# Kernel optimization log

Hardware: AMD Instinct MI355X
Metric: run time of the kernel (lower is better)

Reference implementation:

```python
import jax, jax.numpy as jnp
import numpy as np

EPS = 1e-5

def _layernorm(x, gamma, beta):
    mu = jnp.mean(x, axis=-1, keepdims=True)
    var = jnp.var(x, axis=-1, keepdims=True)
    return (x - mu) * jax.lax.rsqrt(var + EPS) * gamma + beta

def setup_inputs() -> dict:
    key = jax.random.key(0)
    ks = jax.random.split(key, 8)
    B, I, H = 8192, 1024, 1024
    s_w = 1.0 / np.sqrt(I)
    s_u = 1.0 / np.sqrt(H)
    return {
        "x": jax.random.normal(ks[0], (B, I), jnp.float32),
        "h": jax.random.normal(ks[1], (B, H), jnp.float32),
        "c": jax.random.normal(ks[2], (B, H), jnp.float32),
        "W_w": jax.random.uniform(ks[3], (I, 4 * H), jnp.float32, -s_w, s_w),
        "W_b": jax.random.uniform(ks[4], (4 * H,), jnp.float32, -s_w, s_w),
        "U_w": jax.random.uniform(ks[5], (H, 4 * H), jnp.float32, -s_u, s_u),
        "ln_g_gamma": jnp.ones((4 * H,), jnp.float32),
        "ln_g_beta": jnp.zeros((4 * H,), jnp.float32),
        "ln_c_gamma": jnp.ones((H,), jnp.float32),
        "ln_c_beta": jnp.zeros((H,), jnp.float32),
    }

def reference(x, h, c, W_w, W_b, U_w, ln_g_gamma, ln_g_beta, ln_c_gamma, ln_c_beta):
    gates_x = x @ W_w + W_b            # [B, 4H]
    gates_h = h @ U_w                  # [B, 4H]
    gates = gates_x + gates_h + gates_x * gates_h  # multiplicative integration
    gates = _layernorm(gates, ln_g_gamma, ln_g_beta)
    i, f, g, o = jnp.split(gates, 4, axis=-1)
    i = jax.nn.sigmoid(i)
    f = jax.nn.sigmoid(f)
    o = jax.nn.sigmoid(o)
    g = jnp.tanh(g)
    c_new = f * c + i * g
    c_new = _layernorm(c_new, ln_c_gamma, ln_c_beta)
    h_new = o * jnp.tanh(c_new)
    return (h_new, h_new, c_new)
```

## Files before the change

kernel.cpp:

```cpp
#include <hip/hip_runtime.h>
#include <cstdint>


#define MB (1024ull * 1024ull)

typedef short bf16x8 __attribute__((ext_vector_type(8)));
typedef float f32x4  __attribute__((ext_vector_type(4)));

__device__ __forceinline__ bool bf16_mode(const void* g1) {
    return ((const unsigned short*)g1)[0] == 0x3F80u;
}
__device__ __forceinline__ float b2f(unsigned short u) {
    union { unsigned int i; float f; } v; v.i = ((unsigned int)u) << 16; return v.f;
}
__device__ __forceinline__ unsigned short f2b(float f) {
    unsigned int i = __float_as_uint(f);
    unsigned int r = (i + 0x7FFFu + ((i >> 16) & 1u)) >> 16;
    return (unsigned short)r;
}
__device__ __forceinline__ void up4(uint2 v, float* o) {
    o[0] = __uint_as_float(v.x << 16);
    o[1] = __uint_as_float(v.x & 0xFFFF0000u);
    o[2] = __uint_as_float(v.y << 16);
    o[3] = __uint_as_float(v.y & 0xFFFF0000u);
}
__device__ __forceinline__ unsigned int pack2(unsigned short a, unsigned short b) {
    return (unsigned int)a | ((unsigned int)b << 16);
}
__device__ __forceinline__ void ld4(const void* p, size_t idx, bool isbf, float* o) {
    if (isbf) up4(*(const uint2*)((const unsigned short*)p + idx), o);
    else { float4 v = *(const float4*)((const float*)p + idx); o[0]=v.x; o[1]=v.y; o[2]=v.z; o[3]=v.w; }
}
__device__ __forceinline__ float fast_sigmoid(float z) { return 1.f / (1.f + __expf(-z)); }
__device__ __forceinline__ float fast_tanh(float z)    { return 1.f - 2.f / (__expf(2.f * z) + 1.f); }

__device__ __forceinline__ void load_lds16(const unsigned short* g, unsigned short* l) {
    __builtin_amdgcn_global_load_lds(
        (const __attribute__((address_space(1))) unsigned int*)g,
        (__attribute__((address_space(3))) unsigned int*)l,
        16, 0, 0);
}

__global__ __launch_bounds__(256)
void prep_weights(const void* __restrict__ src, const void* __restrict__ g1,
                  unsigned short* __restrict__ dst)
{
    const bool isbf = bf16_mode(g1);
    __shared__ unsigned short tile[64][68];
    const int t  = threadIdx.x;
    const int tx = t & 15;
    const int ty = t >> 4;
    const int bx = blockIdx.x * 64;
    const int by = blockIdx.y * 64;
    if (isbf) {
        const unsigned short* s = (const unsigned short*)src;
#pragma unroll
        for (int it = 0; it < 4; ++it) {
            const int r = ty + it * 16;
            uint2 v = *(const uint2*)(s + (size_t)(by + r) * 4096 + bx + tx * 4);
            tile[r][tx * 4 + 0] = (unsigned short)(v.x & 0xFFFFu);
            tile[r][tx * 4 + 1] = (unsigned short)(v.x >> 16);
            tile[r][tx * 4 + 2] = (unsigned short)(v.y & 0xFFFFu);
            tile[r][tx * 4 + 3] = (unsigned short)(v.y >> 16);
        }
    } else {
        const float* s = (const float*)src;
#pragma unroll
        for (int it = 0; it < 4; ++it) {
            const int r = ty + it * 16;
            float4 v = *(const float4*)(s + (size_t)(by + r) * 4096 + bx + tx * 4);
            tile[r][tx * 4 + 0] = f2b(v.x);
            tile[r][tx * 4 + 1] = f2b(v.y);
            tile[r][tx * 4 + 2] = f2b(v.z);
            tile[r][tx * 4 + 3] = f2b(v.w);
        }
    }
    __syncthreads();
#pragma unroll
    for (int it = 0; it < 4; ++it) {
        const int rn = ty + it * 16;
        const int ck = tx * 4;
        uint2 w;
        w.x = pack2(tile[ck + 0][rn], tile[ck + 1][rn]);
        w.y = pack2(tile[ck + 2][rn], tile[ck + 3][rn]);
        *(uint2*)(dst + (size_t)(bx + rn) * 1024 + by + ck) = w;
    }
}

__global__ __launch_bounds__(256)
void prep_xh(const void* __restrict__ X, const void* __restrict__ Hs,
             const void* __restrict__ g1, void* __restrict__ outb)
{
    if (bf16_mode(g1)) return;
    const float* src = (blockIdx.y == 0) ? (const float*)X : (const float*)Hs;
    unsigned short* dst = (unsigned short*)((char*)outb + (blockIdx.y == 0 ? 48 * MB : 80 * MB));
    const size_t i0 = ((size_t)blockIdx.x * 256 + threadIdx.x) * 8;
    float4 a = *(const float4*)(src + i0);
    float4 b = *(const float4*)(src + i0 + 4);
    uint4 o;
    o.x = pack2(f2b(a.x), f2b(a.y));
    o.y = pack2(f2b(a.z), f2b(a.w));
    o.z = pack2(f2b(b.x), f2b(b.y));
    o.w = pack2(f2b(b.z), f2b(b.w));
    *(uint4*)(dst + i0) = o;
}

#define TM 128
#define TN 128
#define TK 32

__global__ __launch_bounds__(256, 2)
void milstm_gemm(const void* __restrict__ Xraw, const void* __restrict__ Hraw,
                 const void* __restrict__ g1, const void* __restrict__ Wbraw,
                 const void* __restrict__ outb,
                 const unsigned short* __restrict__ Wt,
                 const unsigned short* __restrict__ Ut,
                 unsigned short* __restrict__ G, int m0)
{
    const bool isbf = bf16_mode(g1);
    const unsigned short* X  = isbf ? (const unsigned short*)Xraw
                                    : (const unsigned short*)((const char*)outb + 48 * MB);
    const unsigned short* Hs = isbf ? (const unsigned short*)Hraw
                                    : (const unsigned short*)((const char*)outb + 80 * MB);

    __shared__ __align__(16) unsigned short sAx[TM * TK];
    __shared__ __align__(16) unsigned short sAh[TM * TK];
    __shared__ __align__(16) unsigned short sBw[TN * TK];
    __shared__ __align__(16) unsigned short sBu[TN * TK];

    const int tid  = threadIdx.x;
    const int wave = tid >> 6;
    const int lane = tid & 63;
    const int quad = lane >> 4;
    const int l16  = lane & 15;

    const int bm = blockIdx.y * TM;
    const int bn = blockIdx.x * TN;

    const int wm = (wave & 1) * 64;
    const int wn = (wave >> 1) * 64;

    const int c0   = wave * 2;
    const int srow = lane >> 2;
    const int skb  = (lane & 3) ^ ((srow >> 1) & 3);
    const int scol = skb * 8;

    const unsigned short* px0 = X  + (size_t)(m0 + bm + (c0 + 0) * 16 + srow) * 1024 + scol;
    const unsigned short* px1 = X  + (size_t)(m0 + bm + (c0 + 1) * 16 + srow) * 1024 + scol;
    const unsigned short* ph0 = Hs + (size_t)(m0 + bm + (c0 + 0) * 16 + srow) * 1024 + scol;
    const unsigned short* ph1 = Hs + (size_t)(m0 + bm + (c0 + 1) * 16 + srow) * 1024 + scol;
    const unsigned short* pw0 = Wt + (size_t)(bn + (c0 + 0) * 16 + srow) * 1024 + scol;
    const unsigned short* pw1 = Wt + (size_t)(bn + (c0 + 1) * 16 + srow) * 1024 + scol;
    const unsigned short* pu0 = Ut + (size_t)(bn + (c0 + 0) * 16 + srow) * 1024 + scol;
    const unsigned short* pu1 = Ut + (size_t)(bn + (c0 + 1) * 16 + srow) * 1024 + scol;

    unsigned short* dax0 = sAx + (c0 + 0) * 512;
    unsigned short* dax1 = sAx + (c0 + 1) * 512;
    unsigned short* dah0 = sAh + (c0 + 0) * 512;
    unsigned short* dah1 = sAh + (c0 + 1) * 512;
    unsigned short* dbw0 = sBw + (c0 + 0) * 512;
    unsigned short* dbw1 = sBw + (c0 + 1) * 512;
    unsigned short* dbu0 = sBu + (c0 + 0) * 512;
    unsigned short* dbu1 = sBu + (c0 + 1) * 512;

    const int kread = (quad ^ ((l16 >> 1) & 3)) * 8;

    f32x4 accx[4][4] = {};
    f32x4 acch[4][4] = {};

    for (int k0 = 0; k0 < 1024; k0 += TK) {
        load_lds16(px0 + k0, dax0);
        load_lds16(px1 + k0, dax1);
        load_lds16(ph0 + k0, dah0);
        load_lds16(ph1 + k0, dah1);
        load_lds16(pw0 + k0, dbw0);
        load_lds16(pw1 + k0, dbw1);
        load_lds16(pu0 + k0, dbu0);
        load_lds16(pu1 + k0, dbu1);
        __syncthreads();

        bf16x8 ax[4], ah[4];
#pragma unroll
        for (int mi = 0; mi < 4; ++mi) {
            ax[mi] = *(const bf16x8*)(sAx + (wm + mi * 16 + l16) * TK + kread);
            ah[mi] = *(const bf16x8*)(sAh + (wm + mi * 16 + l16) * TK + kread);
        }
#pragma unroll
        for (int ni = 0; ni < 4; ++ni) {
            bf16x8 bw = *(const bf16x8*)(sBw + (wn + ni * 16 + l16) * TK + kread);
            bf16x8 bu = *(const bf16x8*)(sBu + (wn + ni * 16 + l16) * TK + kread);
#pragma unroll
            for (int mi = 0; mi < 4; ++mi) {
                accx[mi][ni] = __builtin_amdgcn_mfma_f32_16x16x32_bf16(ax[mi], bw, accx[mi][ni], 0, 0, 0);
                acch[mi][ni] = __builtin_amdgcn_mfma_f32_16x16x32_bf16(ah[mi], bu, acch[mi][ni], 0, 0, 0);
            }
        }
        __syncthreads();
    }

#pragma unroll
    for (int ni = 0; ni < 4; ++ni) {
        const int col = bn + wn + ni * 16 + l16;
        const float bias = isbf ? b2f(((const unsigned short*)Wbraw)[col])
                                : ((const float*)Wbraw)[col];
#pragma unroll
        for (int mi = 0; mi < 4; ++mi) {
            const int row0 = bm + wm + mi * 16 + quad * 4;
#pragma unroll
            for (int r = 0; r < 4; ++r) {
                float gx = accx[mi][ni][r] + bias;
                float gh = acch[mi][ni][r];
                float gv = gx + gh + gx * gh;
                G[(size_t)(row0 + r) * 4096 + col] = f2b(gv);
            }
        }
    }
}

__global__ __launch_bounds__(256)
void milstm_cell(const unsigned short* __restrict__ G,
                 const void* __restrict__ C,
                 const void* __restrict__ g1, const void* __restrict__ b1,
                 const void* __restrict__ g2, const void* __restrict__ b2,
                 void* __restrict__ outb, int m0)
{
    const bool isbf = bf16_mode(g1);
    const int lrow = blockIdx.x;
    const int row  = m0 + lrow;
    const int tid  = threadIdx.x;
    const int lane = tid & 63;
    const int wave = tid >> 6;
    const unsigned short* grow = G + (size_t)lrow * 4096;

    __shared__ __align__(16) unsigned short srow[4096];
    __shared__ float red[16];

    float s = 0.f, ss = 0.f;
    const uint4* gv4 = (const uint4*)grow;
#pragma unroll
    for (int u = 0; u < 2; ++u) {
        uint4 v = gv4[tid * 2 + u];
        *(uint4*)(srow + (size_t)(tid * 2 + u) * 8) = v;
        unsigned int w[4] = { v.x, v.y, v.z, v.w };
#pragma unroll
        for (int q = 0; q < 4; ++q) {
            float flo = __uint_as_float(w[q] << 16);
            float fhi = __uint_as_float(w[q] & 0xFFFF0000u);
            s  += flo + fhi;
            ss += flo * flo + fhi * fhi;
        }
    }
#pragma unroll
    for (int off = 32; off > 0; off >>= 1) {
        s  += __shfl_xor(s, off, 64);
        ss += __shfl_xor(ss, off, 64);
    }
    if (lane == 0) { red[wave] = s; red[8 + wave] = ss; }
    __syncthreads();
    s  = red[0] + red[1] + red[2] + red[3];
    ss = red[8] + red[9] + red[10] + red[11];
    const float mu   = s * (1.f / 4096.f);
    const float rstd = rsqrtf(fmaxf(ss * (1.f / 4096.f) - mu * mu, 0.f) + 1e-5f);

    const int j0 = tid * 4;
    float xi[4], xf[4], xg[4], xo[4], cc[4];
    float G1[4], B1[4], ii[4], cn[4], ov[4];

    up4(*(const uint2*)(srow + j0),        xi);
    up4(*(const uint2*)(srow + 1024 + j0), xf);
    up4(*(const uint2*)(srow + 2048 + j0), xg);
    up4(*(const uint2*)(srow + 3072 + j0), xo);
    ld4(C, (size_t)row * 1024 + j0, isbf, cc);

    ld4(g1, j0, isbf, G1); ld4(b1, j0, isbf, B1);
#pragma unroll
    for (int q = 0; q < 4; ++q) ii[q] = fast_sigmoid((xi[q] - mu) * rstd * G1[q] + B1[q]);
    ld4(g1, 1024 + j0, isbf, G1); ld4(b1, 1024 + j0, isbf, B1);
#pragma unroll
    for (int q = 0; q < 4; ++q) xf[q] = fast_sigmoid((xf[q] - mu) * rstd * G1[q] + B1[q]);
    ld4(g1, 2048 + j0, isbf, G1); ld4(b1, 2048 + j0, isbf, B1);
#pragma unroll
    for (int q = 0; q < 4; ++q) xg[q] = fast_tanh((xg[q] - mu) * rstd * G1[q] + B1[q]);
    ld4(g1, 3072 + j0, isbf, G1); ld4(b1, 3072 + j0, isbf, B1);
#pragma unroll
    for (int q = 0; q < 4; ++q) ov[q] = fast_sigmoid((xo[q] - mu) * rstd * G1[q] + B1[q]);
#pragma unroll
    for (int q = 0; q < 4; ++q) cn[q] = xf[q] * cc[q] + ii[q] * xg[q];

    float s2  = cn[0] + cn[1] + cn[2] + cn[3];
    float ss2 = cn[0]*cn[0] + cn[1]*cn[1] + cn[2]*cn[2] + cn[3]*cn[3];
#pragma unroll
    for (int off = 32; off > 0; off >>= 1) {
        s2  += __shfl_xor(s2, off, 64);
        ss2 += __shfl_xor(ss2, off, 64);
    }
    if (lane == 0) { red[4 + wave] = s2; red[12 + wave] = ss2; }
    __syncthreads();
    s2  = red[4]  + red[5]  + red[6]  + red[7];
    ss2 = red[12] + red[13] + red[14] + red[15];
    const float mu2   = s2 * (1.f / 1024.f);
    const float rstd2 = rsqrtf(fmaxf(ss2 * (1.f / 1024.f) - mu2 * mu2, 0.f) + 1e-5f);

    ld4(g2, j0, isbf, G1);
    ld4(b2, j0, isbf, B1);

    float hv[4], cv[4];
#pragma unroll
    for (int q = 0; q < 4; ++q) {
        cv[q] = (cn[q] - mu2) * rstd2 * G1[q] + B1[q];
        hv[q] = ov[q] * fast_tanh(cv[q]);
    }

    const size_t BH = (size_t)8192 * 1024;
    if (isbf) {
        unsigned short* out = (unsigned short*)outb;
        uint2 hb, cb;
        hb.x = pack2(f2b(hv[0]), f2b(hv[1])); hb.y = pack2(f2b(hv[2]), f2b(hv[3]));
        cb.x = pack2(f2b(cv[0]), f2b(cv[1])); cb.y = pack2(f2b(cv[2]), f2b(cv[3]));
        *(uint2*)(out + (size_t)row * 1024 + j0)          = hb;
        *(uint2*)(out + BH + (size_t)row * 1024 + j0)     = hb;
        *(uint2*)(out + 2 * BH + (size_t)row * 1024 + j0) = cb;
    } else {
        float* out = (float*)outb;
        float4 hf = { hv[0], hv[1], hv[2], hv[3] };
        float4 cf = { cv[0], cv[1], cv[2], cv[3] };
        *(float4*)(out + (size_t)row * 1024 + j0)          = hf;
        *(float4*)(out + BH + (size_t)row * 1024 + j0)     = hf;
        *(float4*)(out + 2 * BH + (size_t)row * 1024 + j0) = cf;
    }
}

extern "C" void kernel_launch(void* const* d_in, const int* in_sizes, int n_in,
                              void* d_out, int out_size, void* d_ws, size_t ws_size,
                              hipStream_t stream)
{
    const void* X  = d_in[0];
    const void* Hh = d_in[1];
    const void* C  = d_in[2];
    const void* Ww = d_in[3];
    const void* Wb = d_in[4];
    const void* Uw = d_in[5];
    const void* g1 = d_in[6];
    const void* b1 = d_in[7];
    const void* g2 = d_in[8];
    const void* b2 = d_in[9];

    const bool single = ws_size >= 80 * MB;
    const size_t goff = single ? 64 * MB : 32 * MB;
    unsigned short* G  = (unsigned short*)d_ws;
    unsigned short* Wt = (unsigned short*)((char*)d_ws + goff);
    unsigned short* Ut = (unsigned short*)((char*)d_ws + goff + 8 * MB);

    prep_weights<<<dim3(64, 16), 256, 0, stream>>>(Ww, g1, Wt);
    prep_weights<<<dim3(64, 16), 256, 0, stream>>>(Uw, g1, Ut);
    prep_xh<<<dim3(4096, 2), 256, 0, stream>>>(X, Hh, g1, d_out);

    if (single) {
        milstm_gemm<<<dim3(32, 64), 256, 0, stream>>>(X, Hh, g1, Wb, d_out, Wt, Ut, G, 0);
        milstm_cell<<<dim3(8192), 256, 0, stream>>>(G, C, g1, b1, g2, b2, d_out, 0);
    } else {
        for (int ph = 0; ph < 2; ++ph) {
            const int m0 = ph * 4096;
            milstm_gemm<<<dim3(32, 32), 256, 0, stream>>>(X, Hh, g1, Wb, d_out, Wt, Ut, G, m0);
            milstm_cell<<<dim3(4096), 256, 0, stream>>>(G, C, g1, b1, g2, b2, d_out, m0);
        }
    }
}
```

Measured before the change: 399.7 us.

## Halve GEMM N-tile to raise occupancy and drop LDS staging in cell kernel

The GEMM tile shrinks from 128x128 to 128x64 with 3 blocks per CU. The LDS load assignment is rewritten so each wave issues 6 chunk loads spread across X, H, W and U, and the launch grid doubles in N. The cell kernel now reads each thread's gate slices directly from global memory into registers and preloads all gamma/beta values, removing the shared-memory row copy. This trades lower per-block data reuse (A tiles are reloaded twice as often) for more resident waves and better latency hiding.

```diff
diff --git a/kernel.cpp b/kernel.cpp
--- a/kernel.cpp
+++ b/kernel.cpp
@@ -106,10 +106,10 @@
 }
 
 #define TM 128
-#define TN 128
+#define TN 64
 #define TK 32
 
-__global__ __launch_bounds__(256, 2)
+__global__ __launch_bounds__(256, 3)
 void milstm_gemm(const void* __restrict__ Xraw, const void* __restrict__ Hraw,
                  const void* __restrict__ g1, const void* __restrict__ Wbraw,
                  const void* __restrict__ outb,
@@ -138,45 +138,36 @@
     const int bn = blockIdx.x * TN;
 
     const int wm = (wave & 1) * 64;
-    const int wn = (wave >> 1) * 64;
-
-    const int c0   = wave * 2;
+    const int wn = (wave >> 1) * 32;
+
     const int srow = lane >> 2;
     const int skb  = (lane & 3) ^ ((srow >> 1) & 3);
     const int scol = skb * 8;
 
-    const unsigned short* px0 = X  + (size_t)(m0 + bm + (c0 + 0) * 16 + srow) * 1024 + scol;
-    const unsigned short* px1 = X  + (size_t)(m0 + bm + (c0 + 1) * 16 + srow) * 1024 + scol;
-    const unsigned short* ph0 = Hs + (size_t)(m0 + bm + (c0 + 0) * 16 + srow) * 1024 + scol;
-    const unsigned short* ph1 = Hs + (size_t)(m0 + bm + (c0 + 1) * 16 + srow) * 1024 + scol;
-    const unsigned short* pw0 = Wt + (size_t)(bn + (c0 + 0) * 16 + srow) * 1024 + scol;
-    const unsigned short* pw1 = Wt + (size_t)(bn + (c0 + 1) * 16 + srow) * 1024 + scol;
-    const unsigned short* pu0 = Ut + (size_t)(bn + (c0 + 0) * 16 + srow) * 1024 + scol;
-    const unsigned short* pu1 = Ut + (size_t)(bn + (c0 + 1) * 16 + srow) * 1024 + scol;
-
-    unsigned short* dax0 = sAx + (c0 + 0) * 512;
-    unsigned short* dax1 = sAx + (c0 + 1) * 512;
-    unsigned short* dah0 = sAh + (c0 + 0) * 512;
-    unsigned short* dah1 = sAh + (c0 + 1) * 512;
-    unsigned short* dbw0 = sBw + (c0 + 0) * 512;
-    unsigned short* dbw1 = sBw + (c0 + 1) * 512;
-    unsigned short* dbu0 = sBu + (c0 + 0) * 512;
-    unsigned short* dbu1 = sBu + (c0 + 1) * 512;
+    const unsigned short* gsrc[6];
+    unsigned short* ldst[6];
+#pragma unroll
+    for (int i = 0; i < 6; ++i) {
+        const int c = wave * 6 + i;
+        const unsigned short* base;
+        unsigned short* lbase;
+        int roff, lc;
+        if (c < 8)       { base = X;  lbase = sAx; lc = c;      roff = m0 + bm + lc * 16; }
+        else if (c < 16) { base = Hs; lbase = sAh; lc = c - 8;  roff = m0 + bm + lc * 16; }
+        else if (c < 20) { base = Wt; lbase = sBw; lc = c - 16; roff = bn + lc * 16; }
+        else             { base = Ut; lbase = sBu; lc = c - 20; roff = bn + lc * 16; }
+        gsrc[i] = base + (size_t)(roff + srow) * 1024 + scol;
+        ldst[i] = lbase + lc * 512;
+    }
 
     const int kread = (quad ^ ((l16 >> 1) & 3)) * 8;
 
-    f32x4 accx[4][4] = {};
-    f32x4 acch[4][4] = {};
+    f32x4 accx[4][2] = {};
+    f32x4 acch[4][2] = {};
 
     for (int k0 = 0; k0 < 1024; k0 += TK) {
-        load_lds16(px0 + k0, dax0);
-        load_lds16(px1 + k0, dax1);
-        load_lds16(ph0 + k0, dah0);
-        load_lds16(ph1 + k0, dah1);
-        load_lds16(pw0 + k0, dbw0);
-        load_lds16(pw1 + k0, dbw1);
-        load_lds16(pu0 + k0, dbu0);
-        load_lds16(pu1 + k0, dbu1);
+#pragma unroll
+        for (int i = 0; i < 6; ++i) load_lds16(gsrc[i] + k0, ldst[i]);
         __syncthreads();
 
         bf16x8 ax[4], ah[4];
@@ -186,7 +177,7 @@
             ah[mi] = *(const bf16x8*)(sAh + (wm + mi * 16 + l16) * TK + kread);
         }
 #pragma unroll
-        for (int ni = 0; ni < 4; ++ni) {
+        for (int ni = 0; ni < 2; ++ni) {
             bf16x8 bw = *(const bf16x8*)(sBw + (wn + ni * 16 + l16) * TK + kread);
             bf16x8 bu = *(const bf16x8*)(sBu + (wn + ni * 16 + l16) * TK + kread);
 #pragma unroll
@@ -199,7 +190,7 @@
     }
 
 #pragma unroll
-    for (int ni = 0; ni < 4; ++ni) {
+    for (int ni = 0; ni < 2; ++ni) {
         const int col = bn + wn + ni * 16 + l16;
         const float bias = isbf ? b2f(((const unsigned short*)Wbraw)[col])
                                 : ((const float*)Wbraw)[col];
@@ -231,24 +222,31 @@
     const int lane = tid & 63;
     const int wave = tid >> 6;
     const unsigned short* grow = G + (size_t)lrow * 4096;
-
-    __shared__ __align__(16) unsigned short srow[4096];
+    const int j0 = tid * 4;
+
     __shared__ float red[16];
 
+    uint2 vi = *(const uint2*)(grow + j0);
+    uint2 vf = *(const uint2*)(grow + 1024 + j0);
+    uint2 vg = *(const uint2*)(grow + 2048 + j0);
+    uint2 vo = *(const uint2*)(grow + 3072 + j0);
+    float cc[4];
+    ld4(C, (size_t)row * 1024 + j0, isbf, cc);
+    float Gi[4], Bi[4], Gf[4], Bf[4], Gg[4], Bg[4], Go[4], Bo[4], G2[4], B2[4];
+    ld4(g1, j0, isbf, Gi);          ld4(b1, j0, isbf, Bi);
+    ld4(g1, 1024 + j0, isbf, Gf);   ld4(b1, 1024 + j0, isbf, Bf);
+    ld4(g1, 2048 + j0, isbf, Gg);   ld4(b1, 2048 + j0, isbf, Bg);
+    ld4(g1, 3072 + j0, isbf, Go);   ld4(b1, 3072 + j0, isbf, Bo);
+    ld4(g2, j0, isbf, G2);          ld4(b2, j0, isbf, B2);
+
+    float xi[4], xf[4], xg[4], xo[4];
+    up4(vi, xi); up4(vf, xf); up4(vg, xg); up4(vo, xo);
+
     float s = 0.f, ss = 0.f;
-    const uint4* gv4 = (const uint4*)grow;
-#pragma unroll
-    for (int u = 0; u < 2; ++u) {
-        uint4 v = gv4[tid * 2 + u];
-        *(uint4*)(srow + (size_t)(tid * 2 + u) * 8) = v;
-        unsigned int w[4] = { v.x, v.y, v.z, v.w };
-#pragma unroll
-        for (int q = 0; q < 4; ++q) {
-            float flo = __uint_as_float(w[q] << 16);
-            float fhi = __uint_as_float(w[q] & 0xFFFF0000u);
-            s  += flo + fhi;
-            ss += flo * flo + fhi * fhi;
-        }
+#pragma unroll
+    for (int q = 0; q < 4; ++q) {
+        s  += xi[q] + xf[q] + xg[q] + xo[q];
+        ss += xi[q]*xi[q] + xf[q]*xf[q] + xg[q]*xg[q] + xo[q]*xo[q];
     }
 #pragma unroll
     for (int off = 32; off > 0; off >>= 1) {
@@ -262,30 +260,15 @@
     const float mu   = s * (1.f / 4096.f);
     const float rstd = rsqrtf(fmaxf(ss * (1.f / 4096.f) - mu * mu, 0.f) + 1e-5f);
 
-    const int j0 = tid * 4;
-    float xi[4], xf[4], xg[4], xo[4], cc[4];
-    float G1[4], B1[4], ii[4], cn[4], ov[4];
-
-    up4(*(const uint2*)(srow + j0),        xi);
-    up4(*(const uint2*)(srow + 1024 + j0), xf);
-    up4(*(const uint2*)(srow + 2048 + j0), xg);
-    up4(*(const uint2*)(srow + 3072 + j0), xo);
-    ld4(C, (size_t)row * 1024 + j0, isbf, cc);
-
-    ld4(g1, j0, isbf, G1); ld4(b1, j0, isbf, B1);
-#pragma unroll
-    for (int q = 0; q < 4; ++q) ii[q] = fast_sigmoid((xi[q] - mu) * rstd * G1[q] + B1[q]);
-    ld4(g1, 1024 + j0, isbf, G1); ld4(b1, 1024 + j0, isbf, B1);
-#pragma unroll
-    for (int q = 0; q < 4; ++q) xf[q] = fast_sigmoid((xf[q] - mu) * rstd * G1[q] + B1[q]);
-    ld4(g1, 2048 + j0, isbf, G1); ld4(b1, 2048 + j0, isbf, B1);
-#pragma unroll
-    for (int q = 0; q < 4; ++q) xg[q] = fast_tanh((xg[q] - mu) * rstd * G1[q] + B1[q]);
-    ld4(g1, 3072 + j0, isbf, G1); ld4(b1, 3072 + j0, isbf, B1);
-#pragma unroll
-    for (int q = 0; q < 4; ++q) ov[q] = fast_sigmoid((xo[q] - mu) * rstd * G1[q] + B1[q]);
-#pragma unroll
-    for (int q = 0; q < 4; ++q) cn[q] = xf[q] * cc[q] + ii[q] * xg[q];
+    float ii[4], cn[4], ov[4];
+#pragma unroll
+    for (int q = 0; q < 4; ++q) {
+        ii[q] = fast_sigmoid((xi[q] - mu) * rstd * Gi[q] + Bi[q]);
+        xf[q] = fast_sigmoid((xf[q] - mu) * rstd * Gf[q] + Bf[q]);
+        xg[q] = fast_tanh   ((xg[q] - mu) * rstd * Gg[q] + Bg[q]);
+        ov[q] = fast_sigmoid((xo[q] - mu) * rstd * Go[q] + Bo[q]);
+        cn[q] = xf[q] * cc[q] + ii[q] * xg[q];
+    }
 
     float s2  = cn[0] + cn[1] + cn[2] + cn[3];
     float ss2 = cn[0]*cn[0] + cn[1]*cn[1] + cn[2]*cn[2] + cn[3]*cn[3];
@@ -301,13 +284,10 @@
     const float mu2   = s2 * (1.f / 1024.f);
     const float rstd2 = rsqrtf(fmaxf(ss2 * (1.f / 1024.f) - mu2 * mu2, 0.f) + 1e-5f);
 
-    ld4(g2, j0, isbf, G1);
-    ld4(b2, j0, isbf, B1);
-
     float hv[4], cv[4];
 #pragma unroll
     for (int q = 0; q < 4; ++q) {
-        cv[q] = (cn[q] - mu2) * rstd2 * G1[q] + B1[q];
+        cv[q] = (cn[q] - mu2) * rstd2 * G2[q] + B2[q];
         hv[q] = ov[q] * fast_tanh(cv[q]);
     }
 
@@ -356,12 +336,12 @@
     prep_xh<<<dim3(4096, 2), 256, 0, stream>>>(X, Hh, g1, d_out);
 
     if (single) {
-        milstm_gemm<<<dim3(32, 64), 256, 0, stream>>>(X, Hh, g1, Wb, d_out, Wt, Ut, G, 0);
+        milstm_gemm<<<dim3(64, 64), 256, 0, stream>>>(X, Hh, g1, Wb, d_out, Wt, Ut, G, 0);
         milstm_cell<<<dim3(8192), 256, 0, stream>>>(G, C, g1, b1, g2, b2, d_out, 0);
     } else {
         for (int ph = 0; ph < 2; ++ph) {
             const int m0 = ph * 4096;
-            milstm_gemm<<<dim3(32, 32), 256, 0, stream>>>(X, Hh, g1, Wb, d_out, Wt, Ut, G, m0);
+            milstm_gemm<<<dim3(64, 32), 256, 0, stream>>>(X, Hh, g1, Wb, d_out, Wt, Ut, G, m0);
             milstm_cell<<<dim3(4096), 256, 0, stream>>>(G, C, g1, b1, g2, b2, d_out, m0);
         }
     }
```

After: 458.8 us. +14.8%, slower.
